# Performance work log

Hardware: AMD Instinct MI355X
Metric: run time of the kernel (lower is better)

The kernel has to match this reference:

```python
import jax, jax.numpy as jnp
import numpy as np

LEAKY_ALPHA = 0.2
LN_EPS = 1e-5


def setup_inputs() -> dict:
    key = jax.random.key(0)
    ks = jax.random.split(key, 6)
    B, N, D, R, Hh, hd = 2, 2048, 128, 3, 4, 32  # head_dim = out_dim // num_heads = 128 // 4
    H = jax.random.normal(ks[0], (B, N, D), dtype=jnp.float32)
    A = jax.random.randint(ks[1], (R, B, N, N), 0, 2, dtype=jnp.int32)  # 0/1 adjacency per relation
    w_scale = float(np.sqrt(2.0 / (D + hd)))  # xavier-like
    a_scale = float(np.sqrt(2.0 / (hd + 1)))
    W = jax.random.normal(ks[2], (R, Hh, D, hd), dtype=jnp.float32) * w_scale
    a_src = jax.random.normal(ks[3], (R, Hh, hd), dtype=jnp.float32) * a_scale
    a_dst = jax.random.normal(ks[4], (R, Hh, hd), dtype=jnp.float32) * a_scale
    ln_gamma = jnp.ones((D,), dtype=jnp.float32)
    ln_beta = jnp.zeros((D,), dtype=jnp.float32)
    return {"H": H, "A": A, "W": W, "a_src": a_src, "a_dst": a_dst,
            "ln_gamma": ln_gamma, "ln_beta": ln_beta}


def reference(H, A, W, a_src, a_dst, ln_gamma, ln_beta):
    # H: [B,N,D]; A: [R,B,N,N] int; W: [R,Hh,D,hd]; a_*: [R,Hh,hd]
    R = W.shape[0]
    B, N, D = H.shape
    mask = (A > 0)[:, :, None, :, :]                    # [R,B,1,N,N]
    Wh = jnp.einsum('bnd,rhdf->rbhnf', H, W)             # [R,B,Hh,N,hd]
    e_src = jnp.einsum('rbhnf,rhf->rbhn', Wh, a_src)
    e_dst = jnp.einsum('rbhnf,rhf->rbhn', Wh, a_dst)
    e = e_src[..., :, None] + e_dst[..., None, :]        # [R,B,Hh,N,N]
    e = jax.nn.leaky_relu(e, LEAKY_ALPHA)
    all_false = ~jnp.any(mask, axis=-1, keepdims=True)   # rows with empty neighborhood
    logits = jnp.where(mask, e, -jnp.inf)
    logits = jnp.where(all_false, 0.0, logits)           # avoid NaN on empty rows
    alpha = jax.nn.softmax(logits, axis=-1)
    alpha = jnp.where(all_false, 0.0, alpha)
    # attention-weighted aggregation, mean over relations; -> [B,N,Hh,hd]
    agg = jnp.einsum('rbhij,rbhjf->bihf', alpha, Wh) / R
    out = agg.reshape(B, N, -1)                          # concat heads -> [B,N,out_dim]
    x = H + out                                          # res_proj is Identity (in_dim==out_dim); dropout in eval
    mu = jnp.mean(x, axis=-1, keepdims=True)
    var = jnp.var(x, axis=-1, keepdims=True)
    return (x - mu) / jnp.sqrt(var + LN_EPS) * ln_gamma + ln_beta
```

## Files before the change

kernel.cpp:

```cpp
#include <hip/hip_runtime.h>
#include <hip/hip_bf16.h>

#define RR 3
#define BB 2
#define NN 2048
#define DD 128
#define HH 4
#define HD 32
#define LEAKY 0.2f
#define LN_EPS 1e-5f
#define LOG2E 1.4426950408889634f

using f32x4  = __attribute__((ext_vector_type(4))) float;
using bf16x8 = __attribute__((ext_vector_type(8))) short;

__device__ __forceinline__ void gload_lds16(const void* g, void* l) {
    __builtin_amdgcn_global_load_lds(
        (const __attribute__((address_space(1))) unsigned*)g,
        (__attribute__((address_space(3))) unsigned*)l, 16, 0, 0);
}
__device__ __forceinline__ void gload_lds4(const void* g, void* l) {
    __builtin_amdgcn_global_load_lds(
        (const __attribute__((address_space(1))) unsigned*)g,
        (__attribute__((address_space(3))) unsigned*)l, 4, 0, 0);
}
__device__ __forceinline__ unsigned short bfb(float x) {
    return __builtin_bit_cast(unsigned short, __float2bfloat16(x));
}


__global__ __launch_bounds__(256) void prep_kernel(
    const float* __restrict__ H, const int* __restrict__ A,
    const float* __restrict__ W,
    const float* __restrict__ a_src, const float* __restrict__ a_dst,
    float* __restrict__ es, float* __restrict__ ed,
    __hip_bfloat16* __restrict__ whT, unsigned* __restrict__ bm)
{
    const int bid = blockIdx.x;
    const int t = threadIdx.x;

    if (bid >= 384) {
        const int cb = bid - 384;
        const int wv = cb * 4 + (t >> 6);
        const int lane = t & 63;
        const int4* Ap = (const int4*)A;
#pragma unroll
        for (int e = 0; e < 8; ++e) {
            const long chunk = (long)wv * 8 + e;
            const int4 v = Ap[chunk * 64 + lane];
            const unsigned long long B0 = __ballot(v.x != 0);
            const unsigned long long B1 = __ballot(v.y != 0);
            const unsigned long long B2 = __ballot(v.z != 0);
            const unsigned long long B3 = __ballot(v.w != 0);
            if (lane < 8) {
                const unsigned long long Bq =
                    (lane >= 6) ? B3 : (lane >= 4) ? B2 : (lane >= 2) ? B1 : B0;
                const unsigned word = (lane & 1) ? (unsigned)(Bq >> 32)
                                                 : (unsigned)Bq;
                bm[chunk * 8 + lane] = word;
            }
        }
        return;
    }

    const int rbh = bid >> 4;
    const int nch = bid & 15;
    const int h = rbh & 3;
    const int b = (rbh >> 2) & 1;
    const int r = rbh >> 3;
    const int wi = r * HH + h;
    const int w  = t >> 6;
    const int l  = t & 63;
    const int lr = l & 15;
    const int lg = l >> 4;

    const float* Wp = W + (long)wi * DD * HD;
    bf16x8 afr[2][4];
#pragma unroll
    for (int mt = 0; mt < 2; ++mt)
#pragma unroll
        for (int kt = 0; kt < 4; ++kt)
#pragma unroll
            for (int e = 0; e < 8; ++e)
                afr[mt][kt][e] = (short)bfb(Wp[(kt * 32 + lg * 8 + e) * HD + mt * 16 + lr]);

    float av[2][4], dv[2][4];
#pragma unroll
    for (int mt = 0; mt < 2; ++mt)
#pragma unroll
        for (int reg = 0; reg < 4; ++reg) {
            const int f = mt * 16 + lg * 4 + reg;
            av[mt][reg] = a_src[wi * HD + f] * LOG2E;
            dv[mt][reg] = a_dst[wi * HD + f] * LOG2E;
        }

#pragma unroll
    for (int nt = 0; nt < 2; ++nt) {
        const int ncol = nch * 128 + w * 32 + nt * 16 + lr;
        const float4* hrow4 = (const float4*)(H + ((long)b * NN + ncol) * DD);
        f32x4 acc0 = {0.f, 0.f, 0.f, 0.f};
        f32x4 acc1 = {0.f, 0.f, 0.f, 0.f};
#pragma unroll
        for (int kt = 0; kt < 4; ++kt) {
            float4 h0 = hrow4[kt * 8 + lg * 2];
            float4 h1 = hrow4[kt * 8 + lg * 2 + 1];
            bf16x8 bfr;
            bfr[0] = (short)bfb(h0.x); bfr[1] = (short)bfb(h0.y);
            bfr[2] = (short)bfb(h0.z); bfr[3] = (short)bfb(h0.w);
            bfr[4] = (short)bfb(h1.x); bfr[5] = (short)bfb(h1.y);
            bfr[6] = (short)bfb(h1.z); bfr[7] = (short)bfb(h1.w);
            acc0 = __builtin_amdgcn_mfma_f32_16x16x32_bf16(afr[0][kt], bfr, acc0, 0, 0, 0);
            acc1 = __builtin_amdgcn_mfma_f32_16x16x32_bf16(afr[1][kt], bfr, acc1, 0, 0, 0);
        }
        float s = 0.f, d = 0.f;
#pragma unroll
        for (int reg = 0; reg < 4; ++reg) {
            const int f0 = lg * 4 + reg;
            const int f1 = 16 + lg * 4 + reg;
            whT[((long)rbh * HD + f0) * NN + ncol] = __float2bfloat16(acc0[reg]);
            whT[((long)rbh * HD + f1) * NN + ncol] = __float2bfloat16(acc1[reg]);
            s = fmaf(acc0[reg], av[0][reg], s);
            s = fmaf(acc1[reg], av[1][reg], s);
            d = fmaf(acc0[reg], dv[0][reg], d);
            d = fmaf(acc1[reg], dv[1][reg], d);
        }
        s += __shfl_xor(s, 16); s += __shfl_xor(s, 32);
        d += __shfl_xor(d, 16); d += __shfl_xor(d, 32);
        if (l < 16) {
            es[(long)rbh * NN + ncol] = s;
            ed[(long)rbh * NN + ncol] = d;
        }
    }
}

__global__ __launch_bounds__(256, 3) void gat_attn_kernel(
    const unsigned* __restrict__ bm, const float* __restrict__ es,
    const float* __restrict__ ed, const __hip_bfloat16* __restrict__ whT,
    unsigned* __restrict__ num, float* __restrict__ den)
{
    const int lg = ((int)blockIdx.x % 8) * 96 + (int)blockIdx.x / 8;
    const int jh = lg & 1;
    const int it = (lg >> 1) & 15;
    const int h  = (lg >> 5) & 3;
    const int b  = (lg >> 7) & 1;
    const int r  = lg >> 8;
    const int i0 = it << 7;
    const int tid = threadIdx.x;
    const int w = tid >> 6;
    const int l = tid & 63;
    const int row = l & 15;
    const int kg  = l >> 4;
    const int f31 = l & 31;
    const int kgr = l >> 5;

    __shared__ __align__(16) short    whs[2][4][4][32][8];
    __shared__ __align__(16) unsigned bms[2][4][128];
    __shared__ __align__(16) float    eds[2][4][32];
    __shared__ float red[4];

    const int rbh = (r * BB + b) * HH + h;
    const long rbNN = (long)(r * BB + b) * NN;
    const __hip_bfloat16* whTr = whT + (long)rbh * HD * NN;
    const float* edr = ed + (long)rbh * NN;
    const int jbase = jh * (NN / 2);

#define STAGE(s, nb) do {                                                           \
        const int j0s = jbase + (s) * 128;                                          \
        const int S_ = jh * 8 + (s);                                                \
        const int woff_ = (S_ >> 1) * 8 + (S_ & 1) + w * 2;    \
        gload_lds16(whTr + (long)f31 * NN + j0s + w * 32 + kgr * 8,                 \
                    &whs[nb][w][0][0][0]);                                          \
        gload_lds16(whTr + (long)f31 * NN + j0s + w * 32 + (2 + kgr) * 8,           \
                    &whs[nb][w][2][0][0]);                                          \
        gload_lds4(bm + (rbNN + i0 + l) * 64 + woff_, &bms[nb][w][0]);              \
        gload_lds4(bm + (rbNN + i0 + 64 + l) * 64 + woff_, &bms[nb][w][64]);        \
        if (l < 32) gload_lds4(edr + j0s + w * 32 + l, &eds[nb][w][0]);             \
    } while (0)

    STAGE(0, 0);

    float4 m0 = ((const float4*)edr)[tid * 2];
    float4 m1 = ((const float4*)edr)[tid * 2 + 1];
    float mm = fmaxf(fmaxf(fmaxf(m0.x, m0.y), fmaxf(m0.z, m0.w)),
                     fmaxf(fmaxf(m1.x, m1.y), fmaxf(m1.z, m1.w)));
#pragma unroll
    for (int d = 1; d < 64; d <<= 1) mm = fmaxf(mm, __shfl_xor(mm, d));
    if (l == 0) red[w] = mm;
    __syncthreads();
    const float medf = fmaxf(fmaxf(red[0], red[1]), fmaxf(red[2], red[3]));

    const float esvA = es[(long)rbh * NN + i0 + w * 16 + row];
    const float esvB = es[(long)rbh * NN + i0 + 64 + w * 16 + row];
    const float xA = esvA + medf, xB = esvB + medf;
    const float MA = fmaxf(xA, LEAKY * xA), MB = fmaxf(xB, LEAKY * xB);
    const float uA = esvA - MA, vA = fmaf(LEAKY, esvA, -MA);
    const float uB = esvB - MB, vB = fmaf(LEAKY, esvB, -MB);

    f32x4 acc0A = {0,0,0,0}, acc1A = {0,0,0,0}, accDA = {0,0,0,0};
    f32x4 acc0B = {0,0,0,0}, acc1B = {0,0,0,0}, accDB = {0,0,0,0};
    bf16x8 ones;
#pragma unroll
    for (int i = 0; i < 8; ++i) ones[i] = (short)0x3F80;

    const int kk = kg * 2;
    const int rAi = w * 16 + row, rBi = 64 + w * 16 + row;

    for (int s = 0; s < 8; ++s) {
        const int cb = s & 1, nb = cb ^ 1;
        if (s < 7) {
            STAGE(s + 1, nb);
            asm volatile("s_waitcnt vmcnt(5)" ::: "memory");
        } else {
            asm volatile("s_waitcnt vmcnt(0)" ::: "memory");
        }
        __builtin_amdgcn_s_barrier();
        __builtin_amdgcn_sched_barrier(0);

        unsigned wA[4], wB[4];
#pragma unroll
        for (int q = 0; q < 4; ++q) {
            wA[q] = bms[cb][q][rAi];
            wB[q] = bms[cb][q][rBi];
        }

#pragma unroll
        for (int jc = 0; jc < 4; ++jc) {
            bf16x8 b0 = *(const bf16x8*)&whs[cb][jc][kg][row][0];
            bf16x8 b1 = *(const bf16x8*)&whs[cb][jc][kg][row + 16][0];
            float4 e0 = *(const float4*)&eds[cb][jc][kg * 8];
            float4 e1 = *(const float4*)&eds[cb][jc][kg * 8 + 4];

            unsigned uAq[4], uBq[4];
#pragma unroll
            for (int q = 0; q < 4; ++q) {
                uAq[q] = wA[q] >> (jc * 8 + kk);
                uBq[q] = wB[q] >> (jc * 8 + kk);
            }

            float ev[8];
            ev[0] = e0.x; ev[1] = e0.y; ev[2] = e0.z; ev[3] = e0.w;
            ev[4] = e1.x; ev[5] = e1.y; ev[6] = e1.z; ev[7] = e1.w;

            bf16x8 pA, pB;
#pragma unroll
            for (int c = 0; c < 8; ++c) {
                float pa = __builtin_amdgcn_exp2f(
                    fmaxf(uA + ev[c], fmaf(LEAKY, ev[c], vA)));
                float pb = __builtin_amdgcn_exp2f(
                    fmaxf(uB + ev[c], fmaf(LEAKY, ev[c], vB)));
                const int ma = ((int)(uAq[c & 3] << (31 - (c >> 2)))) >> 31;
                const int mb = ((int)(uBq[c & 3] << (31 - (c >> 2)))) >> 31;
                pa = __uint_as_float(__float_as_uint(pa) & (unsigned)ma);
                pb = __uint_as_float(__float_as_uint(pb) & (unsigned)mb);
                __hip_bfloat16 ha = __float2bfloat16(pa);
                __hip_bfloat16 hb = __float2bfloat16(pb);
                pA[c] = __builtin_bit_cast(short, ha);
                pB[c] = __builtin_bit_cast(short, hb);
            }

            acc0A = __builtin_amdgcn_mfma_f32_16x16x32_bf16(pA, b0, acc0A, 0, 0, 0);
            acc1A = __builtin_amdgcn_mfma_f32_16x16x32_bf16(pA, b1, acc1A, 0, 0, 0);
            accDA = __builtin_amdgcn_mfma_f32_16x16x32_bf16(pA, ones, accDA, 0, 0, 0);
            acc0B = __builtin_amdgcn_mfma_f32_16x16x32_bf16(pB, b0, acc0B, 0, 0, 0);
            acc1B = __builtin_amdgcn_mfma_f32_16x16x32_bf16(pB, b1, acc1B, 0, 0, 0);
            accDB = __builtin_amdgcn_mfma_f32_16x16x32_bf16(pB, ones, accDB, 0, 0, 0);
        }
        __builtin_amdgcn_s_barrier();
        __builtin_amdgcn_sched_barrier(0);
    }
#undef STAGE

    const int fcol = l & 15;
    const int pr = r * 2 + jh;
#pragma unroll
    for (int reg = 0; reg < 4; ++reg) {
        const int orow = (l >> 4) * 4 + reg;
        const long roA = (long)pr * (BB * NN) + (long)b * NN + i0 + w * 16 + orow;
        const long roB = roA + 64;
        const unsigned wa = (unsigned)bfb(acc0A[reg]) | ((unsigned)bfb(acc1A[reg]) << 16);
        const unsigned wb_ = (unsigned)bfb(acc0B[reg]) | ((unsigned)bfb(acc1B[reg]) << 16);
        num[roA * 64 + h * 16 + fcol] = wa;
        num[roB * 64 + h * 16 + fcol] = wb_;
        if (fcol == 0) {
            den[roA * HH + h] = accDA[reg];
            den[roB * HH + h] = accDB[reg];
        }
    }
}

__global__ __launch_bounds__(256) void finalize_kernel(
    const float* __restrict__ H, const unsigned* __restrict__ num,
    const float* __restrict__ den,
    const float* __restrict__ gamma, const float* __restrict__ beta,
    float* __restrict__ out)
{
    const int w = threadIdx.x >> 6;
    const int l = threadIdx.x & 63;
    const long row = (long)blockIdx.x * 4 + w;
    const int hh = l >> 4, cc = l & 15;
    const int c_lo = hh * 32 + cc, c_hi = c_lo + 16;
    const float hx = H[row * DD + c_lo];
    const float hy = H[row * DD + c_hi];

    float ax = 0.f, ay = 0.f;
#pragma unroll
    for (int r = 0; r < RR; ++r) {
        float dsum = 0.f, nx = 0.f, ny = 0.f;
#pragma unroll
        for (int j = 0; j < 2; ++j) {
            const long ro = (long)(r * 2 + j) * (BB * NN) + row;
            dsum += den[ro * HH + hh];
            const unsigned wv = num[ro * 64 + l];
            nx += __uint_as_float(wv << 16);
            ny += __uint_as_float(wv & 0xffff0000u);
        }
        const float inv = (dsum > 0.f) ? 1.0f / dsum : 0.0f;
        ax = fmaf(nx, inv, ax);
        ay = fmaf(ny, inv, ay);
    }
    const float x0 = hx + ax * (1.0f / RR);
    const float x1 = hy + ay * (1.0f / RR);
    float s = x0 + x1, q = x0 * x0 + x1 * x1;
#pragma unroll
    for (int m = 1; m < 64; m <<= 1) {
        s += __shfl_xor(s, m);
        q += __shfl_xor(q, m);
    }
    const float mu  = s * (1.0f / DD);
    const float var = q * (1.0f / DD) - mu * mu;
    const float inv = rsqrtf(var + LN_EPS);
    out[row * DD + c_lo] = (x0 - mu) * inv * gamma[c_lo] + beta[c_lo];
    out[row * DD + c_hi] = (x1 - mu) * inv * gamma[c_hi] + beta[c_hi];
}

extern "C" void kernel_launch(void* const* d_in, const int* in_sizes, int n_in,
                              void* d_out, int out_size, void* d_ws, size_t ws_size,
                              hipStream_t stream)
{
    const float* H      = (const float*)d_in[0];
    const int*   A      = (const int*)d_in[1];
    const float* W      = (const float*)d_in[2];
    const float* a_src  = (const float*)d_in[3];
    const float* a_dst  = (const float*)d_in[4];
    const float* gamma  = (const float*)d_in[5];
    const float* beta   = (const float*)d_in[6];
    float* out = (float*)d_out;

    char* ws = (char*)d_ws;
    unsigned* num = (unsigned*)ws;               ws += (size_t)RR * 2 * BB * NN * 64 * 4;
    float* den = (float*)ws;                     ws += (size_t)RR * 2 * BB * NN * HH * 4;
    float* es  = (float*)ws;                     ws += (size_t)RR * BB * HH * NN * 4;
    float* ed  = (float*)ws;                     ws += (size_t)RR * BB * HH * NN * 4;
    __hip_bfloat16* whT = (__hip_bfloat16*)ws;   ws += (size_t)RR * BB * HH * HD * NN * 2;
    unsigned* bmask = (unsigned*)ws;             ws += (size_t)RR * BB * NN * (NN / 32) * 4;

    prep_kernel<<<384 + RR * BB * NN * (NN / 32) / 256, 256, 0, stream>>>(
        H, A, W, a_src, a_dst, es, ed, whT, bmask);
    gat_attn_kernel<<<RR * BB * HH * 16 * 2, 256, 0, stream>>>(bmask, es, ed, whT, num, den);
    finalize_kernel<<<BB * NN / 4, 256, 0, stream>>>(H, num, den, gamma, beta, out);
}
```

Before: 66.14 us.

## Fuse prep, attention and finalize into one cooperative persistent kernel

Adds a single cooperative kernel of 768 blocks that runs the mask bit-packing, the Wh projection with its score precompute, the masked softmax aggregation and the LayerNorm finalize as phases separated by grid-wide syncs. This removes two kernel launches and the gaps between them, and lets the mask packing be spread across all blocks. In exchange it pays for two grid barriers and runs at occupancy 3 blocks per CU via launch bounds. If cooperative launch or the occupancy check fails, it falls back to the old three-kernel path.

```diff
diff --git a/kernel.cpp b/kernel.cpp
--- a/kernel.cpp
+++ b/kernel.cpp
@@ -1,5 +1,8 @@
 #include <hip/hip_runtime.h>
 #include <hip/hip_bf16.h>
+#include <hip/hip_cooperative_groups.h>
+
+namespace cg = cooperative_groups;
 
 #define RR 3
 #define BB 2
@@ -28,6 +31,312 @@
     return __builtin_bit_cast(unsigned short, __float2bfloat16(x));
 }
 
+
+__global__ __launch_bounds__(256, 3) void fused_kernel(
+    const float* __restrict__ H, const int* __restrict__ A,
+    const float* __restrict__ W,
+    const float* __restrict__ a_src, const float* __restrict__ a_dst,
+    const float* __restrict__ gamma, const float* __restrict__ beta,
+    float* __restrict__ out,
+    float* __restrict__ es, float* __restrict__ ed,
+    __hip_bfloat16* __restrict__ whT, unsigned* __restrict__ bm,
+    unsigned* __restrict__ num, float* __restrict__ den)
+{
+    __shared__ __align__(16) short    whs[2][4][4][32][8];
+    __shared__ __align__(16) unsigned bms[2][4][128];
+    __shared__ __align__(16) float    eds[2][4][32];
+    __shared__ float red[4];
+
+    const int bid = blockIdx.x;
+    const int t = threadIdx.x;
+    const int w = t >> 6;
+    const int l = t & 63;
+
+    {
+        const int g = bid * 4 + w;
+        const int4* Ap = (const int4*)A;
+#pragma unroll 1
+        for (int rr = 0; rr < 4; ++rr) {
+            const long crow = (long)g * 4 + rr;
+#pragma unroll
+            for (int e = 0; e < 8; ++e) {
+                const long chunk = crow * 8 + e;
+                const int4 v = Ap[chunk * 64 + l];
+                const unsigned long long B0 = __ballot(v.x != 0);
+                const unsigned long long B1 = __ballot(v.y != 0);
+                const unsigned long long B2 = __ballot(v.z != 0);
+                const unsigned long long B3 = __ballot(v.w != 0);
+                if (l < 8) {
+                    const unsigned long long Bq =
+                        (l >= 6) ? B3 : (l >= 4) ? B2 : (l >= 2) ? B1 : B0;
+                    bm[chunk * 8 + l] = (l & 1) ? (unsigned)(Bq >> 32)
+                                                : (unsigned)Bq;
+                }
+            }
+        }
+    }
+
+    if (bid < 384) {
+        const int rbh = bid >> 4;
+        const int nch = bid & 15;
+        const int h = rbh & 3;
+        const int b = (rbh >> 2) & 1;
+        const int r = rbh >> 3;
+        const int wi = r * HH + h;
+        const int lr = l & 15;
+        const int lg = l >> 4;
+
+        const float* Wp = W + (long)wi * DD * HD;
+        bf16x8 afr[2][4];
+#pragma unroll
+        for (int mt = 0; mt < 2; ++mt)
+#pragma unroll
+            for (int kt = 0; kt < 4; ++kt)
+#pragma unroll
+                for (int e = 0; e < 8; ++e)
+                    afr[mt][kt][e] = (short)bfb(Wp[(kt * 32 + lg * 8 + e) * HD + mt * 16 + lr]);
+
+        float av[2][4], dv[2][4];
+#pragma unroll
+        for (int mt = 0; mt < 2; ++mt)
+#pragma unroll
+            for (int reg = 0; reg < 4; ++reg) {
+                const int f = mt * 16 + lg * 4 + reg;
+                av[mt][reg] = a_src[wi * HD + f] * LOG2E;
+                dv[mt][reg] = a_dst[wi * HD + f] * LOG2E;
+            }
+
+#pragma unroll
+        for (int nt = 0; nt < 2; ++nt) {
+            const int ncol = nch * 128 + w * 32 + nt * 16 + lr;
+            const float4* hrow4 = (const float4*)(H + ((long)b * NN + ncol) * DD);
+            f32x4 acc0 = {0.f, 0.f, 0.f, 0.f};
+            f32x4 acc1 = {0.f, 0.f, 0.f, 0.f};
+#pragma unroll
+            for (int kt = 0; kt < 4; ++kt) {
+                float4 h0 = hrow4[kt * 8 + lg * 2];
+                float4 h1 = hrow4[kt * 8 + lg * 2 + 1];
+                bf16x8 bfr;
+                bfr[0] = (short)bfb(h0.x); bfr[1] = (short)bfb(h0.y);
+                bfr[2] = (short)bfb(h0.z); bfr[3] = (short)bfb(h0.w);
+                bfr[4] = (short)bfb(h1.x); bfr[5] = (short)bfb(h1.y);
+                bfr[6] = (short)bfb(h1.z); bfr[7] = (short)bfb(h1.w);
+                acc0 = __builtin_amdgcn_mfma_f32_16x16x32_bf16(afr[0][kt], bfr, acc0, 0, 0, 0);
+                acc1 = __builtin_amdgcn_mfma_f32_16x16x32_bf16(afr[1][kt], bfr, acc1, 0, 0, 0);
+            }
+            float s = 0.f, d = 0.f;
+#pragma unroll
+            for (int reg = 0; reg < 4; ++reg) {
+                const int f0 = lg * 4 + reg;
+                const int f1 = 16 + lg * 4 + reg;
+                whT[((long)rbh * HD + f0) * NN + ncol] = __float2bfloat16(acc0[reg]);
+                whT[((long)rbh * HD + f1) * NN + ncol] = __float2bfloat16(acc1[reg]);
+                s = fmaf(acc0[reg], av[0][reg], s);
+                s = fmaf(acc1[reg], av[1][reg], s);
+                d = fmaf(acc0[reg], dv[0][reg], d);
+                d = fmaf(acc1[reg], dv[1][reg], d);
+            }
+            s += __shfl_xor(s, 16); s += __shfl_xor(s, 32);
+            d += __shfl_xor(d, 16); d += __shfl_xor(d, 32);
+            if (l < 16) {
+                es[(long)rbh * NN + ncol] = s;
+                ed[(long)rbh * NN + ncol] = d;
+            }
+        }
+    }
+
+    __threadfence();
+    cg::this_grid().sync();
+    __threadfence();
+    __builtin_amdgcn_sched_barrier(0);
+
+    {
+        const int lgs = (bid % 8) * 96 + bid / 8;
+        const int jh = lgs & 1;
+        const int it = (lgs >> 1) & 15;
+        const int h  = (lgs >> 5) & 3;
+        const int b  = (lgs >> 7) & 1;
+        const int r  = lgs >> 8;
+        const int i0 = it << 7;
+        const int row = l & 15;
+        const int kg  = l >> 4;
+        const int f31 = l & 31;
+        const int kgr = l >> 5;
+
+        const int rbh = (r * BB + b) * HH + h;
+        const long rbNN = (long)(r * BB + b) * NN;
+        const __hip_bfloat16* whTr = whT + (long)rbh * HD * NN;
+        const float* edr = ed + (long)rbh * NN;
+        const int jbase = jh * (NN / 2);
+
+#define STAGEF(s, nb) do {                                                          \
+        const int j0s = jbase + (s) * 128;                                          \
+        const int S_ = jh * 8 + (s);                                                \
+        const int woff_ = (S_ >> 1) * 8 + (S_ & 1) + w * 2;                         \
+        gload_lds16(whTr + (long)f31 * NN + j0s + w * 32 + kgr * 8,                 \
+                    &whs[nb][w][0][0][0]);                                          \
+        gload_lds16(whTr + (long)f31 * NN + j0s + w * 32 + (2 + kgr) * 8,           \
+                    &whs[nb][w][2][0][0]);                                          \
+        gload_lds4(bm + (rbNN + i0 + l) * 64 + woff_, &bms[nb][w][0]);              \
+        gload_lds4(bm + (rbNN + i0 + 64 + l) * 64 + woff_, &bms[nb][w][64]);        \
+        if (l < 32) gload_lds4(edr + j0s + w * 32 + l, &eds[nb][w][0]);             \
+    } while (0)
+
+        STAGEF(0, 0);
+
+        float4 m0 = ((const float4*)edr)[t * 2];
+        float4 m1 = ((const float4*)edr)[t * 2 + 1];
+        float mm = fmaxf(fmaxf(fmaxf(m0.x, m0.y), fmaxf(m0.z, m0.w)),
+                         fmaxf(fmaxf(m1.x, m1.y), fmaxf(m1.z, m1.w)));
+#pragma unroll
+        for (int d = 1; d < 64; d <<= 1) mm = fmaxf(mm, __shfl_xor(mm, d));
+        if (l == 0) red[w] = mm;
+        __syncthreads();
+        const float medf = fmaxf(fmaxf(red[0], red[1]), fmaxf(red[2], red[3]));
+
+        const float esvA = es[(long)rbh * NN + i0 + w * 16 + row];
+        const float esvB = es[(long)rbh * NN + i0 + 64 + w * 16 + row];
+        const float xA = esvA + medf, xB = esvB + medf;
+        const float MA = fmaxf(xA, LEAKY * xA), MB = fmaxf(xB, LEAKY * xB);
+        const float uA = esvA - MA, vA = fmaf(LEAKY, esvA, -MA);
+        const float uB = esvB - MB, vB = fmaf(LEAKY, esvB, -MB);
+
+        f32x4 acc0A = {0,0,0,0}, acc1A = {0,0,0,0}, accDA = {0,0,0,0};
+        f32x4 acc0B = {0,0,0,0}, acc1B = {0,0,0,0}, accDB = {0,0,0,0};
+        bf16x8 ones;
+#pragma unroll
+        for (int i = 0; i < 8; ++i) ones[i] = (short)0x3F80;
+
+        const int kk = kg * 2;
+        const int rAi = w * 16 + row, rBi = 64 + w * 16 + row;
+
+        for (int s = 0; s < 8; ++s) {
+            const int cb = s & 1, nb = cb ^ 1;
+            if (s < 7) {
+                STAGEF(s + 1, nb);
+                asm volatile("s_waitcnt vmcnt(5)" ::: "memory");
+            } else {
+                asm volatile("s_waitcnt vmcnt(0)" ::: "memory");
+            }
+            __builtin_amdgcn_s_barrier();
+            __builtin_amdgcn_sched_barrier(0);
+
+            unsigned wA[4], wB[4];
+#pragma unroll
+            for (int q = 0; q < 4; ++q) {
+                wA[q] = bms[cb][q][rAi];
+                wB[q] = bms[cb][q][rBi];
+            }
+
+#pragma unroll
+            for (int jc = 0; jc < 4; ++jc) {
+                bf16x8 b0 = *(const bf16x8*)&whs[cb][jc][kg][row][0];
+                bf16x8 b1 = *(const bf16x8*)&whs[cb][jc][kg][row + 16][0];
+                float4 e0 = *(const float4*)&eds[cb][jc][kg * 8];
+                float4 e1 = *(const float4*)&eds[cb][jc][kg * 8 + 4];
+
+                unsigned uAq[4], uBq[4];
+#pragma unroll
+                for (int q = 0; q < 4; ++q) {
+                    uAq[q] = wA[q] >> (jc * 8 + kk);
+                    uBq[q] = wB[q] >> (jc * 8 + kk);
+                }
+
+                float ev[8];
+                ev[0] = e0.x; ev[1] = e0.y; ev[2] = e0.z; ev[3] = e0.w;
+                ev[4] = e1.x; ev[5] = e1.y; ev[6] = e1.z; ev[7] = e1.w;
+
+                bf16x8 pA, pB;
+#pragma unroll
+                for (int c = 0; c < 8; ++c) {
+                    float pa = __builtin_amdgcn_exp2f(
+                        fmaxf(uA + ev[c], fmaf(LEAKY, ev[c], vA)));
+                    float pb = __builtin_amdgcn_exp2f(
+                        fmaxf(uB + ev[c], fmaf(LEAKY, ev[c], vB)));
+                    const int ma = ((int)(uAq[c & 3] << (31 - (c >> 2)))) >> 31;
+                    const int mb = ((int)(uBq[c & 3] << (31 - (c >> 2)))) >> 31;
+                    pa = __uint_as_float(__float_as_uint(pa) & (unsigned)ma);
+                    pb = __uint_as_float(__float_as_uint(pb) & (unsigned)mb);
+                    __hip_bfloat16 ha = __float2bfloat16(pa);
+                    __hip_bfloat16 hb = __float2bfloat16(pb);
+                    pA[c] = __builtin_bit_cast(short, ha);
+                    pB[c] = __builtin_bit_cast(short, hb);
+                }
+
+                acc0A = __builtin_amdgcn_mfma_f32_16x16x32_bf16(pA, b0, acc0A, 0, 0, 0);
+                acc1A = __builtin_amdgcn_mfma_f32_16x16x32_bf16(pA, b1, acc1A, 0, 0, 0);
+                accDA = __builtin_amdgcn_mfma_f32_16x16x32_bf16(pA, ones, accDA, 0, 0, 0);
+                acc0B = __builtin_amdgcn_mfma_f32_16x16x32_bf16(pB, b0, acc0B, 0, 0, 0);
+                acc1B = __builtin_amdgcn_mfma_f32_16x16x32_bf16(pB, b1, acc1B, 0, 0, 0);
+                accDB = __builtin_amdgcn_mfma_f32_16x16x32_bf16(pB, ones, accDB, 0, 0, 0);
+            }
+            __builtin_amdgcn_s_barrier();
+            __builtin_amdgcn_sched_barrier(0);
+        }
+#undef STAGEF
+
+        const int fcol = l & 15;
+        const int pr = r * 2 + jh;
+#pragma unroll
+        for (int reg = 0; reg < 4; ++reg) {
+            const int orow = (l >> 4) * 4 + reg;
+            const long roA = (long)pr * (BB * NN) + (long)b * NN + i0 + w * 16 + orow;
+            const long roB = roA + 64;
+            const unsigned wa = (unsigned)bfb(acc0A[reg]) | ((unsigned)bfb(acc1A[reg]) << 16);
+            const unsigned wb_ = (unsigned)bfb(acc0B[reg]) | ((unsigned)bfb(acc1B[reg]) << 16);
+            num[roA * 64 + h * 16 + fcol] = wa;
+            num[roB * 64 + h * 16 + fcol] = wb_;
+            if (fcol == 0) {
+                den[roA * HH + h] = accDA[reg];
+                den[roB * HH + h] = accDB[reg];
+            }
+        }
+    }
+
+    __threadfence();
+    cg::this_grid().sync();
+    __threadfence();
+    __builtin_amdgcn_sched_barrier(0);
+
+#pragma unroll 1
+    for (int g4 = bid; g4 < BB * NN / 4; g4 += 768) {
+        const long row = (long)g4 * 4 + w;
+        const int hh = l >> 4, cc = l & 15;
+        const int c_lo = hh * 32 + cc, c_hi = c_lo + 16;
+        const float hx = H[row * DD + c_lo];
+        const float hy = H[row * DD + c_hi];
+
+        float ax = 0.f, ay = 0.f;
+#pragma unroll
+        for (int r = 0; r < RR; ++r) {
+            float dsum = 0.f, nx = 0.f, ny = 0.f;
+#pragma unroll
+            for (int j = 0; j < 2; ++j) {
+                const long ro = (long)(r * 2 + j) * (BB * NN) + row;
+                dsum += den[ro * HH + hh];
+                const unsigned wv = num[ro * 64 + l];
+                nx += __uint_as_float(wv << 16);
+                ny += __uint_as_float(wv & 0xffff0000u);
+            }
+            const float inv = (dsum > 0.f) ? 1.0f / dsum : 0.0f;
+            ax = fmaf(nx, inv, ax);
+            ay = fmaf(ny, inv, ay);
+        }
+        const float x0 = hx + ax * (1.0f / RR);
+        const float x1 = hy + ay * (1.0f / RR);
+        float s = x0 + x1, q = x0 * x0 + x1 * x1;
+#pragma unroll
+        for (int m = 1; m < 64; m <<= 1) {
+            s += __shfl_xor(s, m);
+            q += __shfl_xor(q, m);
+        }
+        const float mu  = s * (1.0f / DD);
+        const float var = q * (1.0f / DD) - mu * mu;
+        const float inv = rsqrtf(var + LN_EPS);
+        out[row * DD + c_lo] = (x0 - mu) * inv * gamma[c_lo] + beta[c_lo];
+        out[row * DD + c_hi] = (x1 - mu) * inv * gamma[c_hi] + beta[c_hi];
+    }
+}
 
 __global__ __launch_bounds__(256) void prep_kernel(
     const float* __restrict__ H, const int* __restrict__ A,
@@ -55,9 +364,8 @@
             if (lane < 8) {
                 const unsigned long long Bq =
                     (lane >= 6) ? B3 : (lane >= 4) ? B2 : (lane >= 2) ? B1 : B0;
-                const unsigned word = (lane & 1) ? (unsigned)(Bq >> 32)
-                                                 : (unsigned)Bq;
-                bm[chunk * 8 + lane] = word;
+                bm[chunk * 8 + lane] = (lane & 1) ? (unsigned)(Bq >> 32)
+                                                  : (unsigned)Bq;
             }
         }
         return;
@@ -167,7 +475,7 @@
 #define STAGE(s, nb) do {                                                           \
         const int j0s = jbase + (s) * 128;                                          \
         const int S_ = jh * 8 + (s);                                                \
-        const int woff_ = (S_ >> 1) * 8 + (S_ & 1) + w * 2;    \
+        const int woff_ = (S_ >> 1) * 8 + (S_ & 1) + w * 2;                         \
         gload_lds16(whTr + (long)f31 * NN + j0s + w * 32 + kgr * 8,                 \
                     &whs[nb][w][0][0][0]);                                          \
         gload_lds16(whTr + (long)f31 * NN + j0s + w * 32 + (2 + kgr) * 8,           \
@@ -354,6 +662,18 @@
     __hip_bfloat16* whT = (__hip_bfloat16*)ws;   ws += (size_t)RR * BB * HH * HD * NN * 2;
     unsigned* bmask = (unsigned*)ws;             ws += (size_t)RR * BB * NN * (NN / 32) * 4;
 
+    int mb = 0;
+    hipError_t oe = hipOccupancyMaxActiveBlocksPerMultiprocessor(&mb, fused_kernel, 256, 0);
+    if (oe == hipSuccess && mb >= 3) {
+        void* args[] = { (void*)&H, (void*)&A, (void*)&W, (void*)&a_src, (void*)&a_dst,
+                         (void*)&gamma, (void*)&beta, (void*)&out,
+                         (void*)&es, (void*)&ed, (void*)&whT, (void*)&bmask,
+                         (void*)&num, (void*)&den };
+        if (hipLaunchCooperativeKernel((void*)fused_kernel, dim3(768), dim3(256),
+                                       args, 0, stream) == hipSuccess)
+            return;
+    }
+
     prep_kernel<<<384 + RR * BB * NN * (NN / 32) / 256, 256, 0, stream>>>(
         H, A, W, a_src, a_dst, es, ed, whT, bmask);
     gat_attn_kernel<<<RR * BB * HH * 16 * 2, 256, 0, stream>>>(bmask, es, ed, whT, num, den);
```

Result: no change. 66.77 us (+0.9%).
